# Optimization experiments

Hardware: AMD Instinct MI355X
Metric: run time of the kernel (lower is better)

The kernel has to match this reference:

```python
import jax, jax.numpy as jnp
import numpy as np

HEAD = 8
D = 128
GIN = 256
GOUT = 256
N = 50000
E = 800000


def gt_layer(edge_index, embeds, qT, kT, vT, ln_s, ln_b):
    rows, cols = edge_index[0], edge_index[1]
    n, d = embeds.shape
    hd = d // HEAD
    rowE = embeds[rows]  # [E, d]
    colE = embeds[cols]  # [E, d]
    q = (rowE @ qT).reshape(-1, HEAD, hd)
    k = (colE @ kT).reshape(-1, HEAD, hd)
    v = (colE @ vT).reshape(-1, HEAD, hd)
    att = jnp.clip(jnp.einsum('ehd,ehd->eh', q, k), -10.0, 10.0)
    expAtt = jnp.exp(att)  # [E, H]
    attNorm = jax.ops.segment_sum(expAtt, rows, num_segments=n)[rows]  # scatter-softmax denom
    att = expAtt / (attNorm + 1e-8)
    res = (att[..., None] * v).reshape(-1, d)  # [E, d]
    agg = jax.ops.segment_sum(res, rows, num_segments=n)  # [n, d]
    out = agg + embeds
    mu = jnp.mean(out, axis=-1, keepdims=True)
    var = jnp.mean((out - mu) ** 2, axis=-1, keepdims=True)
    return (out - mu) / jnp.sqrt(var + 1e-6) * ln_s + ln_b


def setup_inputs() -> dict:
    key = jax.random.key(0)
    ks = jax.random.split(key, 16)
    def xavier(k, shape):
        lim = np.sqrt(6.0 / (shape[0] + shape[1]))
        return jax.random.uniform(k, shape, jnp.float32, -lim, lim)
    inp = {
        'x': jax.random.normal(ks[0], (N, GIN), jnp.float32),
        'edge_index': jax.random.randint(ks[1], (2, E), 0, N, jnp.int64),
        'W_P_w': xavier(ks[2], (GIN, D)),
        'W_P_b': jnp.zeros((D,), jnp.float32),
        'W_pos': jax.random.uniform(ks[3], (1, D), jnp.float32, -0.02, 0.02),
        'q1': xavier(ks[4], (D, D)), 'k1': xavier(ks[5], (D, D)), 'v1': xavier(ks[6], (D, D)),
        'ln1_s': jnp.ones((D,), jnp.float32), 'ln1_b': jnp.zeros((D,), jnp.float32),
        'q2': xavier(ks[7], (D, D)), 'k2': xavier(ks[8], (D, D)), 'v2': xavier(ks[9], (D, D)),
        'ln2_s': jnp.ones((D,), jnp.float32), 'ln2_b': jnp.zeros((D,), jnp.float32),
        'inv_w': xavier(ks[10], (D, GOUT)),
        'inv_b': jnp.zeros((GOUT,), jnp.float32),
    }
    return inp


def reference(x, edge_index, W_P_w, W_P_b, W_pos, q1, k1, v1, ln1_s, ln1_b,
              q2, k2, v2, ln2_s, ln2_b, inv_w, inv_b):
    z = x @ W_P_w + W_P_b          # W_P linear: [N, D]
    embeds = z + W_pos              # if_pos; dropout is identity in eval
    embeds = gt_layer(edge_index, embeds, q1, k1, v1, ln1_s, ln1_b)
    embeds = gt_layer(edge_index, embeds, q2, k2, v2, ln2_s, ln2_b)
    return embeds @ inv_w + inv_b   # [N, GOUT]
```

## Files before the change

kernel.cpp:

```cpp
#include <hip/hip_runtime.h>
#include <hip/hip_bf16.h>

#define HEADS 8
#define DIM 128

typedef short s8v __attribute__((ext_vector_type(8)));
typedef float f4v __attribute__((ext_vector_type(4)));

__device__ __forceinline__ float bf2f(unsigned int lo16) {
    union { unsigned int i; float f; } v; v.i = lo16 << 16; return v.f;
}
__device__ __forceinline__ unsigned short f2bf(float f) {
    __hip_bfloat16 h = __float2bfloat16(f);
    return *reinterpret_cast<unsigned short*>(&h);
}
__device__ __forceinline__ int imin(int a, int b) { return a < b ? a : b; }

template<int CTRL>
__device__ __forceinline__ float dpp_add_f(float x) {
    int y = __builtin_amdgcn_update_dpp(0, __float_as_int(x), CTRL, 0xF, 0xF, true);
    return x + __int_as_float(y);
}

#if __has_builtin(__builtin_amdgcn_exp2f)
#define fast_exp2(x) __builtin_amdgcn_exp2f(x)
#else
#define fast_exp2(x) __expf(0.6931471805599453f * (x))
#endif

__global__ __launch_bounds__(256) void setup_k(const void* __restrict__ ei, int n2, int E,
                                               int* __restrict__ out, int* __restrict__ deg) {
    __shared__ int cnt;
    const unsigned int* w = (const unsigned int*)ei;
    if (threadIdx.x == 0) cnt = 0;
    __syncthreads();
    if (w[2 * threadIdx.x + 1] == 0u) atomicAdd(&cnt, 1);
    __syncthreads();
    const bool is64 = cnt > 192;
    int i = blockIdx.x * 256 + threadIdx.x;
    if (i < n2) {
        int v = is64 ? (int)((const long long*)ei)[i] : ((const int*)ei)[i];
        out[i] = v;
        if (i < E) atomicAdd(&deg[v], 1);
    }
}

__global__ void scan1_k(const int* __restrict__ deg, int n,
                        int* __restrict__ incl, int* __restrict__ blkSums) {
    __shared__ int s[256];
    int i = blockIdx.x * 256 + threadIdx.x;
    int v = (i < n) ? deg[i] : 0;
    s[threadIdx.x] = v;
    __syncthreads();
    for (int off = 1; off < 256; off <<= 1) {
        int t = (threadIdx.x >= off) ? s[threadIdx.x - off] : 0;
        __syncthreads();
        s[threadIdx.x] += t;
        __syncthreads();
    }
    if (i < n) incl[i] = s[threadIdx.x];
    if (threadIdx.x == 255) blkSums[blockIdx.x] = s[255];
}

__global__ void scan2_k(int* __restrict__ blkSums, int nb) {
    __shared__ int s[256];
    int v = (threadIdx.x < nb) ? blkSums[threadIdx.x] : 0;
    s[threadIdx.x] = v;
    __syncthreads();
    for (int off = 1; off < 256; off <<= 1) {
        int t = (threadIdx.x >= off) ? s[threadIdx.x - off] : 0;
        __syncthreads();
        s[threadIdx.x] += t;
        __syncthreads();
    }
    if (threadIdx.x < nb) blkSums[threadIdx.x] = s[threadIdx.x] - v;
}

__global__ void scan3_k(const int* __restrict__ incl, const int* __restrict__ deg,
                        const int* __restrict__ blkOff, int n,
                        int* __restrict__ rowPtr, int* __restrict__ cursor) {
    int i = blockIdx.x * 256 + threadIdx.x;
    if (i < n) {
        int inc = incl[i] + blkOff[blockIdx.x];
        rowPtr[i + 1] = inc;
        cursor[i] = inc - deg[i];
    }
    if (i == 0) rowPtr[0] = 0;
}

__global__ void scatter_k(const int* __restrict__ rows, const int* __restrict__ cols, int E,
                          int* __restrict__ cursor, int* __restrict__ colIdx) {
    int e = blockIdx.x * 256 + threadIdx.x;
    if (e < E) {
        int pos = atomicAdd(&cursor[rows[e]], 1);
        colIdx[pos] = cols[e];
    }
}

__global__ __launch_bounds__(256) void build_all_wfrag_k(
    const float* __restrict__ Wp, const float* __restrict__ q1, const float* __restrict__ k1,
    const float* __restrict__ v1, const float* __restrict__ q2, const float* __restrict__ k2,
    const float* __restrict__ v2, const float* __restrict__ invw,
    unsigned short* __restrict__ wfragP, unsigned short* __restrict__ wfragQKV1,
    unsigned short* __restrict__ wfragQKV2, unsigned short* __restrict__ wfragO)
{
    const int b = blockIdx.x;
    const float* W; unsigned short* dst; int Kd, Nd, ncomp, fb;
    const int split = 2;
    if (b < 32) { W = Wp; dst = wfragP; Kd = 256; Nd = 128; ncomp = 2; fb = b; }
    else if (b < 128) {
        int j = (b - 32) >> 4, r = (b - 32) & 15;
        const float* ws[6] = { q1, k1, v1, q2, k2, v2 };
        W = ws[j];
        dst = ((j < 3) ? wfragQKV1 : wfragQKV2) + (size_t)(j % 3) * 2 * 128 * 128;
        Kd = 128; Nd = 128; ncomp = 2; fb = r;
    } else { W = invw; dst = wfragO; Kd = 128; Nd = 256; ncomp = 1; fb = b - 128; }

    int f = fb * 256 + threadIdx.x;
    int KS = Kd >> 5;
    int perPhase = (Nd / 16 / split) * KS * 64;
    if (f >= ncomp * split * perPhase) return;
    int comp = f / (split * perPhase);
    int r1 = f - comp * split * perPhase;
    int p = r1 / perPhase;
    int r = r1 - p * perPhase;
    int nt = r / (KS * 64);
    int r2 = r - nt * KS * 64;
    int ks = r2 >> 6, lane = r2 & 63;
    int n = p * (Nd / split) + nt * 16 + (lane & 15);
    int k0 = ks * 32 + (lane >> 4) * 8;
    unsigned short tmp[8];
#pragma unroll
    for (int j = 0; j < 8; j++) {
        float w = W[(size_t)(k0 + j) * Nd + n];
        unsigned short hi = f2bf(w);
        tmp[j] = (comp == 0) ? hi : f2bf(w - bf2f(hi));
    }
#pragma unroll
    for (int j = 0; j < 8; j++) dst[(size_t)f * 8 + j] = tmp[j];
}

__global__ __launch_bounds__(256) void proj_k(
    const float* __restrict__ A, const unsigned short* __restrict__ wfrag,
    const float* __restrict__ b0, const float* __restrict__ b1,
    unsigned short* __restrict__ ehi, unsigned short* __restrict__ elo, int M)
{
    constexpr int KD = 256, KS = 8, NTp = 4;
    constexpr int FRp = NTp * KS * 64;
    const int lane = threadIdx.x & 63;
    const int m16 = lane & 15, q4 = lane >> 4;
    const int phase = blockIdx.y;
    const int pairIdx = blockIdx.x * 4 + (threadIdx.x >> 6);
    const int nPairs = (M + 31) >> 5;
    if (pairIdx >= nPairs) return;

    const int row0 = pairIdx * 32;
    const int rA0 = imin(row0 + m16, M - 1);
    const int rA1 = imin(row0 + 16 + m16, M - 1);

    f4v acc0[NTp], acc1[NTp];
#pragma unroll
    for (int nt = 0; nt < NTp; nt++) { acc0[nt] = (f4v){0,0,0,0}; acc1[nt] = (f4v){0,0,0,0}; }

    for (int ks = 0; ks < KS; ks++) {
        const f4v* pa0 = (const f4v*)(A + (size_t)rA0 * KD + ks * 32 + q4 * 8);
        const f4v* pa1 = (const f4v*)(A + (size_t)rA1 * KD + ks * 32 + q4 * 8);
        f4v xa = pa0[0], xb = pa0[1], ya = pa1[0], yb = pa1[1];
        s8v a0h, a0l, a1h, a1l;
#pragma unroll
        for (int j = 0; j < 4; j++) {
            unsigned short h;
            h = f2bf(xa[j]); a0h[j] = (short)h; a0l[j] = (short)f2bf(xa[j] - bf2f(h));
            h = f2bf(xb[j]); a0h[4 + j] = (short)h; a0l[4 + j] = (short)f2bf(xb[j] - bf2f(h));
            h = f2bf(ya[j]); a1h[j] = (short)h; a1l[j] = (short)f2bf(ya[j] - bf2f(h));
            h = f2bf(yb[j]); a1h[4 + j] = (short)h; a1l[4 + j] = (short)f2bf(yb[j] - bf2f(h));
        }
#pragma unroll
        for (int nt = 0; nt < NTp; nt++) {
            const size_t fi = ((size_t)(nt * KS + ks) * 64 + lane) * 8;
            s8v bh = *(const s8v*)(wfrag + ((size_t)(0 * 2 + phase) * FRp) * 8 + fi);
            s8v bl = *(const s8v*)(wfrag + ((size_t)(1 * 2 + phase) * FRp) * 8 + fi);
            acc0[nt] = __builtin_amdgcn_mfma_f32_16x16x32_bf16(a0h, bh, acc0[nt], 0, 0, 0);
            acc0[nt] = __builtin_amdgcn_mfma_f32_16x16x32_bf16(a0h, bl, acc0[nt], 0, 0, 0);
            acc0[nt] = __builtin_amdgcn_mfma_f32_16x16x32_bf16(a0l, bh, acc0[nt], 0, 0, 0);
            acc1[nt] = __builtin_amdgcn_mfma_f32_16x16x32_bf16(a1h, bh, acc1[nt], 0, 0, 0);
            acc1[nt] = __builtin_amdgcn_mfma_f32_16x16x32_bf16(a1h, bl, acc1[nt], 0, 0, 0);
            acc1[nt] = __builtin_amdgcn_mfma_f32_16x16x32_bf16(a1l, bh, acc1[nt], 0, 0, 0);
        }
    }

#pragma unroll
    for (int nt = 0; nt < NTp; nt++) {
        const int col = phase * 64 + nt * 16 + m16;
        const float bias = b0[col] + b1[col];
#pragma unroll
        for (int r = 0; r < 4; r++) {
            const int gr0 = row0 + q4 * 4 + r;
            if (gr0 < M) {
                float v = acc0[nt][r] + bias;
                unsigned short h = f2bf(v);
                ehi[(size_t)gr0 * DIM + col] = h;
                elo[(size_t)gr0 * DIM + col] = f2bf(v - bf2f(h));
            }
            const int gr1 = gr0 + 16;
            if (gr1 < M && row0 + 16 < M) {
                float v = acc1[nt][r] + bias;
                unsigned short h = f2bf(v);
                ehi[(size_t)gr1 * DIM + col] = h;
                elo[(size_t)gr1 * DIM + col] = f2bf(v - bf2f(h));
            }
        }
    }
}

__global__ __launch_bounds__(256) void qkv_k(
    const unsigned short* __restrict__ ehi, const unsigned short* __restrict__ elo,
    const unsigned short* __restrict__ wfrag,
    float* __restrict__ Qb, unsigned short* __restrict__ KVb, int M)
{
    constexpr int KS = 4, NTp = 4;
    constexpr int FRp = NTp * KS * 64;
    constexpr int MATFR = 4 * FRp;
    const int lane = threadIdx.x & 63;
    const int m16 = lane & 15, q4 = lane >> 4;
    const int phase = blockIdx.y;
    const int pairIdx = blockIdx.x * 4 + (threadIdx.x >> 6);
    const int nPairs = (M + 31) >> 5;
    if (pairIdx >= nPairs) return;

    const int row0 = pairIdx * 32;
    const int rA0 = imin(row0 + m16, M - 1);
    const int rA1 = imin(row0 + 16 + m16, M - 1);

    s8v a0h[KS], a0l[KS], a1h[KS], a1l[KS];
#pragma unroll
    for (int ks = 0; ks < KS; ks++) {
        a0h[ks] = *(const s8v*)(ehi + (size_t)rA0 * DIM + ks * 32 + q4 * 8);
        a0l[ks] = *(const s8v*)(elo + (size_t)rA0 * DIM + ks * 32 + q4 * 8);
        a1h[ks] = *(const s8v*)(ehi + (size_t)rA1 * DIM + ks * 32 + q4 * 8);
        a1l[ks] = *(const s8v*)(elo + (size_t)rA1 * DIM + ks * 32 + q4 * 8);
    }

    f4v aQ0[NTp], aQ1[NTp], aK0[NTp], aK1[NTp], aV0[NTp], aV1[NTp];
#pragma unroll
    for (int nt = 0; nt < NTp; nt++) {
        aQ0[nt] = (f4v){0,0,0,0}; aQ1[nt] = (f4v){0,0,0,0};
        aK0[nt] = (f4v){0,0,0,0}; aK1[nt] = (f4v){0,0,0,0};
        aV0[nt] = (f4v){0,0,0,0}; aV1[nt] = (f4v){0,0,0,0};
    }

#pragma unroll
    for (int ks = 0; ks < KS; ks++) {
#pragma unroll
        for (int nt = 0; nt < NTp; nt++) {
            const size_t fi = ((size_t)(nt * KS + ks) * 64 + lane) * 8;
            s8v qh = *(const s8v*)(wfrag + (size_t)(0 * MATFR + (0 * 2 + phase) * FRp) * 8 + fi);
            s8v ql = *(const s8v*)(wfrag + (size_t)(0 * MATFR + (1 * 2 + phase) * FRp) * 8 + fi);
            s8v kh = *(const s8v*)(wfrag + (size_t)(1 * MATFR + (0 * 2 + phase) * FRp) * 8 + fi);
            s8v kl = *(const s8v*)(wfrag + (size_t)(1 * MATFR + (1 * 2 + phase) * FRp) * 8 + fi);
            s8v vh = *(const s8v*)(wfrag + (size_t)(2 * MATFR + (0 * 2 + phase) * FRp) * 8 + fi);
            aQ0[nt] = __builtin_amdgcn_mfma_f32_16x16x32_bf16(a0h[ks], qh, aQ0[nt], 0, 0, 0);
            aQ0[nt] = __builtin_amdgcn_mfma_f32_16x16x32_bf16(a0h[ks], ql, aQ0[nt], 0, 0, 0);
            aQ0[nt] = __builtin_amdgcn_mfma_f32_16x16x32_bf16(a0l[ks], qh, aQ0[nt], 0, 0, 0);
            aQ1[nt] = __builtin_amdgcn_mfma_f32_16x16x32_bf16(a1h[ks], qh, aQ1[nt], 0, 0, 0);
            aQ1[nt] = __builtin_amdgcn_mfma_f32_16x16x32_bf16(a1h[ks], ql, aQ1[nt], 0, 0, 0);
            aQ1[nt] = __builtin_amdgcn_mfma_f32_16x16x32_bf16(a1l[ks], qh, aQ1[nt], 0, 0, 0);
            aK0[nt] = __builtin_amdgcn_mfma_f32_16x16x32_bf16(a0h[ks], kh, aK0[nt], 0, 0, 0);
            aK0[nt] = __builtin_amdgcn_mfma_f32_16x16x32_bf16(a0h[ks], kl, aK0[nt], 0, 0, 0);
            aK0[nt] = __builtin_amdgcn_mfma_f32_16x16x32_bf16(a0l[ks], kh, aK0[nt], 0, 0, 0);
            aK1[nt] = __builtin_amdgcn_mfma_f32_16x16x32_bf16(a1h[ks], kh, aK1[nt], 0, 0, 0);
            aK1[nt] = __builtin_amdgcn_mfma_f32_16x16x32_bf16(a1h[ks], kl, aK1[nt], 0, 0, 0);
            aK1[nt] = __builtin_amdgcn_mfma_f32_16x16x32_bf16(a1l[ks], kh, aK1[nt], 0, 0, 0);
            aV0[nt] = __builtin_amdgcn_mfma_f32_16x16x32_bf16(a0h[ks], vh, aV0[nt], 0, 0, 0);
            aV0[nt] = __builtin_amdgcn_mfma_f32_16x16x32_bf16(a0l[ks], vh, aV0[nt], 0, 0, 0);
            aV1[nt] = __builtin_amdgcn_mfma_f32_16x16x32_bf16(a1h[ks], vh, aV1[nt], 0, 0, 0);
            aV1[nt] = __builtin_amdgcn_mfma_f32_16x16x32_bf16(a1l[ks], vh, aV1[nt], 0, 0, 0);
        }
    }

#pragma unroll
    for (int nt = 0; nt < NTp; nt++) {
        const int col = phase * 64 + nt * 16 + m16;
#pragma unroll
        for (int r = 0; r < 4; r++) {
            const int gr0 = row0 + q4 * 4 + r;
            if (gr0 < M) {
                Qb[(size_t)gr0 * DIM + col] = aQ0[nt][r];
                KVb[(size_t)gr0 * 256 + col] = f2bf(aK0[nt][r]);
                KVb[(size_t)gr0 * 256 + 128 + col] = f2bf(aV0[nt][r]);
            }
            const int gr1 = gr0 + 16;
            if (gr1 < M && row0 + 16 < M) {
                Qb[(size_t)gr1 * DIM + col] = aQ1[nt][r];
                KVb[(size_t)gr1 * 256 + col] = f2bf(aK1[nt][r]);
                KVb[(size_t)gr1 * 256 + 128 + col] = f2bf(aV1[nt][r]);
            }
        }
    }
}

__global__ __launch_bounds__(256) void outproj_k(
    const unsigned short* __restrict__ ehi, const unsigned short* __restrict__ elo,
    const unsigned short* __restrict__ wfrag, const float* __restrict__ b0,
    float* __restrict__ Out, int M)
{
    constexpr int KS = 4, NTp = 8, NOUT = 256;
    constexpr int FRp = NTp * KS * 64;
    const int lane = threadIdx.x & 63;
    const int m16 = lane & 15, q4 = lane >> 4;
    const int phase = blockIdx.y;
    const int pairIdx = blockIdx.x * 4 + (threadIdx.x >> 6);
    const int nPairs = (M + 31) >> 5;
    if (pairIdx >= nPairs) return;

    const int row0 = pairIdx * 32;
    const int rA0 = imin(row0 + m16, M - 1);
    const int rA1 = imin(row0 + 16 + m16, M - 1);

    s8v a0h[KS], a0l[KS], a1h[KS], a1l[KS];
#pragma unroll
    for (int ks = 0; ks < KS; ks++) {
        a0h[ks] = *(const s8v*)(ehi + (size_t)rA0 * DIM + ks * 32 + q4 * 8);
        a0l[ks] = *(const s8v*)(elo + (size_t)rA0 * DIM + ks * 32 + q4 * 8);
        a1h[ks] = *(const s8v*)(ehi + (size_t)rA1 * DIM + ks * 32 + q4 * 8);
        a1l[ks] = *(const s8v*)(elo + (size_t)rA1 * DIM + ks * 32 + q4 * 8);
    }

    f4v acc0[NTp], acc1[NTp];
#pragma unroll
    for (int nt = 0; nt < NTp; nt++) { acc0[nt] = (f4v){0,0,0,0}; acc1[nt] = (f4v){0,0,0,0}; }

#pragma unroll
    for (int ks = 0; ks < KS; ks++) {
#pragma unroll
        for (int nt = 0; nt < NTp; nt++) {
            s8v b = *(const s8v*)(wfrag + ((size_t)phase * FRp + (size_t)(nt * KS + ks) * 64 + lane) * 8);
            acc0[nt] = __builtin_amdgcn_mfma_f32_16x16x32_bf16(a0h[ks], b, acc0[nt], 0, 0, 0);
            acc0[nt] = __builtin_amdgcn_mfma_f32_16x16x32_bf16(a0l[ks], b, acc0[nt], 0, 0, 0);
            acc1[nt] = __builtin_amdgcn_mfma_f32_16x16x32_bf16(a1h[ks], b, acc1[nt], 0, 0, 0);
            acc1[nt] = __builtin_amdgcn_mfma_f32_16x16x32_bf16(a1l[ks], b, acc1[nt], 0, 0, 0);
        }
    }

#pragma unroll
    for (int nt = 0; nt < NTp; nt++) {
        const int col = phase * 128 + nt * 16 + m16;
        const float bias = b0[col];
#pragma unroll
        for (int r = 0; r < 4; r++) {
            const int gr0 = row0 + q4 * 4 + r;
            if (gr0 < M) Out[(size_t)gr0 * NOUT + col] = acc0[nt][r] + bias;
            const int gr1 = gr0 + 16;
            if (gr1 < M && row0 + 16 < M) Out[(size_t)gr1 * NOUT + col] = acc1[nt][r] + bias;
        }
    }
}

__global__ __launch_bounds__(256) void agg_k(
    const float* __restrict__ Q, const unsigned short* __restrict__ KV,
    const int* __restrict__ rowPtr, const int* __restrict__ colIdx,
    const float* __restrict__ ln_s, const float* __restrict__ ln_b,
    unsigned short* __restrict__ ehi, unsigned short* __restrict__ elo, int n)
{
    const int node = blockIdx.x * 4 + (threadIdx.x >> 6);
    if (node >= n) return;
    const int lane = threadIdx.x & 63;
    const int d = lane * 2;

    constexpr float LOG2E = 1.4426950408889634f;
    constexpr float CLAMP = 10.0f * LOG2E;

    const float2 qraw = *(const float2*)(Q + (size_t)node * DIM + d);
    const float qx = qraw.x * LOG2E, qy = qraw.y * LOG2E;
    const unsigned int rh = *(const unsigned int*)(ehi + (size_t)node * DIM + d);
    const unsigned int rl = *(const unsigned int*)(elo + (size_t)node * DIM + d);
    const float r0 = bf2f(rh & 0xffffu) + bf2f(rl & 0xffffu);
    const float r1 = bf2f(rh >> 16) + bf2f(rl >> 16);

    const int e0 = rowPtr[node], e1 = rowPtr[node + 1];
    float acc0 = 0.f, acc1 = 0.f, den = 0.f;

    if (e1 > e0) {
        unsigned int kA[4], vA[4], kB[4], vB[4];
#define LOADC(karr, varr, base_)                                        \
        {                                                               \
            _Pragma("unroll")                                           \
            for (int j = 0; j < 4; j++) {                               \
                int idx = (base_) + j;                                  \
                int cc = colIdx[idx < e1 ? idx : e1 - 1];               \
                size_t off = (size_t)cc * 256 + d;                      \
                karr[j] = *(const unsigned int*)(KV + off);             \
                varr[j] = *(const unsigned int*)(KV + off + 128);       \
            }                                                           \
        }
#define COMP(karr, varr, base_)                                         \
        {                                                               \
            _Pragma("unroll")                                           \
            for (int j = 0; j < 4; j++) {                               \
                if ((base_) + j < e1) {                                 \
                    float p = qx * bf2f(karr[j] & 0xffffu)              \
                            + qy * bf2f(karr[j] >> 16);                 \
                    p = dpp_add_f<0xB1>(p);                   \
                    p = dpp_add_f<0x4E>(p);                   \
                    p = dpp_add_f<0x141>(p);    \
                    p = fminf(fmaxf(p, -CLAMP), CLAMP);                 \
                    float w = fast_exp2(p);                             \
                    den += w;                                           \
                    acc0 += w * bf2f(varr[j] & 0xffffu);                \
                    acc1 += w * bf2f(varr[j] >> 16);                    \
                }                                                       \
            }                                                           \
        }
        int base = e0;
        LOADC(kA, vA, base)
        while (base < e1) {
            int nxt = base + 4;
            if (nxt < e1) LOADC(kB, vB, nxt)
            COMP(kA, vA, base)
            base = nxt;
            if (base >= e1) break;
            int nxt2 = base + 4;
            if (nxt2 < e1) LOADC(kA, vA, nxt2)
            COMP(kB, vB, base)
            base = nxt2;
        }
#undef LOADC
#undef COMP
    }
    const float inv = 1.f / (den + 1e-8f);
    const float o0 = acc0 * inv + r0;
    const float o1 = acc1 * inv + r1;

    float s = o0 + o1, s2 = o0 * o0 + o1 * o1;
#pragma unroll
    for (int m = 1; m < 64; m <<= 1) {
        s  += __shfl_xor(s, m);
        s2 += __shfl_xor(s2, m);
    }
    const float mu = s * (1.f / 128.f);
    const float var = s2 * (1.f / 128.f) - mu * mu;
    const float rs = rsqrtf(var + 1e-6f);
    const float y0 = (o0 - mu) * rs * ln_s[d] + ln_b[d];
    const float y1 = (o1 - mu) * rs * ln_s[d + 1] + ln_b[d + 1];
    const unsigned short h0 = f2bf(y0), h1 = f2bf(y1);
    const unsigned short l0 = f2bf(y0 - bf2f(h0)), l1 = f2bf(y1 - bf2f(h1));
    *(unsigned int*)(ehi + (size_t)node * DIM + d) = (unsigned int)h0 | ((unsigned int)h1 << 16);
    *(unsigned int*)(elo + (size_t)node * DIM + d) = (unsigned int)l0 | ((unsigned int)l1 << 16);
}

extern "C" void kernel_launch(void* const* d_in, const int* in_sizes, int n_in,
                              void* d_out, int out_size, void* d_ws, size_t ws_size,
                              hipStream_t stream)
{
    const float* x    = (const float*)d_in[0];
    const void*  ei   = d_in[1];
    const float* Wp   = (const float*)d_in[2];
    const float* Wpb  = (const float*)d_in[3];
    const float* Wpos = (const float*)d_in[4];
    const float* q1   = (const float*)d_in[5];
    const float* k1   = (const float*)d_in[6];
    const float* v1   = (const float*)d_in[7];
    const float* l1s  = (const float*)d_in[8];
    const float* l1b  = (const float*)d_in[9];
    const float* q2   = (const float*)d_in[10];
    const float* k2   = (const float*)d_in[11];
    const float* v2   = (const float*)d_in[12];
    const float* l2s  = (const float*)d_in[13];
    const float* l2b  = (const float*)d_in[14];
    const float* invw = (const float*)d_in[15];
    const float* invb = (const float*)d_in[16];

    const int N = in_sizes[0] / 256;
    const int E = in_sizes[1] / 2;

    char* p = (char*)d_ws;
    auto carve = [&](size_t bytes) -> void* {
        void* r = (void*)p;
        p += (bytes + 255) & ~(size_t)255;
        return r;
    };
    unsigned short* ehi = (unsigned short*)carve((size_t)N * DIM * 2);
    unsigned short* elo = (unsigned short*)carve((size_t)N * DIM * 2);
    float*          Qb  = (float*)carve((size_t)N * DIM * 4);
    unsigned short* KVb = (unsigned short*)carve((size_t)N * 256 * 2);
    int*   deg    = (int*)carve((size_t)N * 4);
    int*   incl   = (int*)carve((size_t)N * 4);
    int*   blkS   = (int*)carve(1024);
    int*   rowPtr = (int*)carve((size_t)(N + 1) * 4);
    int*   cursor = (int*)carve((size_t)N * 4);
    int*   colIdx = (int*)carve((size_t)E * 4);
    int*   rc     = (int*)carve((size_t)2 * E * 4);
    unsigned short* wfragP    = (unsigned short*)carve((size_t)2 * 256 * 128 * 2);
    unsigned short* wfragQKV1 = (unsigned short*)carve((size_t)3 * 2 * 128 * 128 * 2);
    unsigned short* wfragQKV2 = (unsigned short*)carve((size_t)3 * 2 * 128 * 128 * 2);
    unsigned short* wfragO    = (unsigned short*)carve((size_t)128 * 256 * 2);

    int* rows = rc;
    int* cols = rc + E;

    const int nb  = (N + 255) / 256;
    const int ebl = (E + 255) / 256;
    const int nPairs = (N + 31) / 32;
    const dim3 ggrid((nPairs + 3) / 4, 2);

    hipMemsetAsync(deg, 0, (size_t)N * 4, stream);
    setup_k<<<(2 * E + 255) / 256, 256, 0, stream>>>(ei, 2 * E, E, rc, deg);
    scan1_k<<<nb, 256, 0, stream>>>(deg, N, incl, blkS);
    scan2_k<<<1, 256, 0, stream>>>(blkS, nb);
    scan3_k<<<nb, 256, 0, stream>>>(incl, deg, blkS, N, rowPtr, cursor);
    scatter_k<<<ebl, 256, 0, stream>>>(rows, cols, E, cursor, colIdx);

    build_all_wfrag_k<<<144, 256, 0, stream>>>(Wp, q1, k1, v1, q2, k2, v2, invw,
                                               wfragP, wfragQKV1, wfragQKV2, wfragO);

    proj_k<<<ggrid, 256, 0, stream>>>(x, wfragP, Wpb, Wpos, ehi, elo, N);

    qkv_k<<<ggrid, 256, 0, stream>>>(ehi, elo, wfragQKV1, Qb, KVb, N);
    agg_k<<<(N + 3) / 4, 256, 0, stream>>>(Qb, KVb, rowPtr, colIdx, l1s, l1b, ehi, elo, N);

    qkv_k<<<ggrid, 256, 0, stream>>>(ehi, elo, wfragQKV2, Qb, KVb, N);
    agg_k<<<(N + 3) / 4, 256, 0, stream>>>(Qb, KVb, rowPtr, colIdx, l2s, l2b, ehi, elo, N);

    outproj_k<<<ggrid, 256, 0, stream>>>(ehi, elo, wfragO, invb, (float*)d_out, N);
}
```

Before: 496.0 us.

## Interleave K/V layout, merge proj phases, and use DPP wave reduction

The K and V bf16 values for each column are now interleaved in one 32-bit word. The aggregation kernel can then fetch K and V together with a single 8-byte load per lane per neighbor, instead of two separate 4-byte loads 256 bytes apart. The projection kernel now computes all 128 output columns in one wave rather than splitting the work across two grid phases, so the input x is read and converted to bf16 only once. The aggregation loop replaces per-edge branches with a masked weight, and the layer-norm reduction uses DPP row operations plus readlane instead of shuffle xor. The merged projection doubles the accumulator registers per wave, which could reduce occupancy.

Result: no change. 488.0 us (-1.6%).

```diff
diff --git a/kernel.cpp b/kernel.cpp
--- a/kernel.cpp
+++ b/kernel.cpp
@@ -20,6 +20,16 @@
 __device__ __forceinline__ float dpp_add_f(float x) {
     int y = __builtin_amdgcn_update_dpp(0, __float_as_int(x), CTRL, 0xF, 0xF, true);
     return x + __int_as_float(y);
+}
+
+__device__ __forceinline__ float wave_allsum(float x) {
+    x = dpp_add_f<0x111>(x);
+    x = dpp_add_f<0x112>(x);
+    x = dpp_add_f<0x114>(x);
+    x = dpp_add_f<0x118>(x);
+    x = dpp_add_f<0x142>(x);
+    x = dpp_add_f<0x143>(x);
+    return __int_as_float(__builtin_amdgcn_readlane(__float_as_int(x), 63));
 }
 
 #if __has_builtin(__builtin_amdgcn_exp2f)
@@ -145,11 +155,10 @@
     const float* __restrict__ b0, const float* __restrict__ b1,
     unsigned short* __restrict__ ehi, unsigned short* __restrict__ elo, int M)
 {
-    constexpr int KD = 256, KS = 8, NTp = 4;
-    constexpr int FRp = NTp * KS * 64;
+    constexpr int KD = 256, KS = 8, NT = 8;
+    constexpr int FRp = 4 * KS * 64;
     const int lane = threadIdx.x & 63;
     const int m16 = lane & 15, q4 = lane >> 4;
-    const int phase = blockIdx.y;
     const int pairIdx = blockIdx.x * 4 + (threadIdx.x >> 6);
     const int nPairs = (M + 31) >> 5;
     if (pairIdx >= nPairs) return;
@@ -158,9 +167,9 @@
     const int rA0 = imin(row0 + m16, M - 1);
     const int rA1 = imin(row0 + 16 + m16, M - 1);
 
-    f4v acc0[NTp], acc1[NTp];
-#pragma unroll
-    for (int nt = 0; nt < NTp; nt++) { acc0[nt] = (f4v){0,0,0,0}; acc1[nt] = (f4v){0,0,0,0}; }
+    f4v acc0[NT], acc1[NT];
+#pragma unroll
+    for (int g = 0; g < NT; g++) { acc0[g] = (f4v){0,0,0,0}; acc1[g] = (f4v){0,0,0,0}; }
 
     for (int ks = 0; ks < KS; ks++) {
         const f4v* pa0 = (const f4v*)(A + (size_t)rA0 * KD + ks * 32 + q4 * 8);
@@ -176,35 +185,36 @@
             h = f2bf(yb[j]); a1h[4 + j] = (short)h; a1l[4 + j] = (short)f2bf(yb[j] - bf2f(h));
         }
 #pragma unroll
-        for (int nt = 0; nt < NTp; nt++) {
+        for (int g = 0; g < NT; g++) {
+            const int p = g >> 2, nt = g & 3;
             const size_t fi = ((size_t)(nt * KS + ks) * 64 + lane) * 8;
-            s8v bh = *(const s8v*)(wfrag + ((size_t)(0 * 2 + phase) * FRp) * 8 + fi);
-            s8v bl = *(const s8v*)(wfrag + ((size_t)(1 * 2 + phase) * FRp) * 8 + fi);
-            acc0[nt] = __builtin_amdgcn_mfma_f32_16x16x32_bf16(a0h, bh, acc0[nt], 0, 0, 0);
-            acc0[nt] = __builtin_amdgcn_mfma_f32_16x16x32_bf16(a0h, bl, acc0[nt], 0, 0, 0);
-            acc0[nt] = __builtin_amdgcn_mfma_f32_16x16x32_bf16(a0l, bh, acc0[nt], 0, 0, 0);
-            acc1[nt] = __builtin_amdgcn_mfma_f32_16x16x32_bf16(a1h, bh, acc1[nt], 0, 0, 0);
-            acc1[nt] = __builtin_amdgcn_mfma_f32_16x16x32_bf16(a1h, bl, acc1[nt], 0, 0, 0);
-            acc1[nt] = __builtin_amdgcn_mfma_f32_16x16x32_bf16(a1l, bh, acc1[nt], 0, 0, 0);
-        }
-    }
-
-#pragma unroll
-    for (int nt = 0; nt < NTp; nt++) {
-        const int col = phase * 64 + nt * 16 + m16;
+            s8v bh = *(const s8v*)(wfrag + ((size_t)(0 * 2 + p) * FRp) * 8 + fi);
+            s8v bl = *(const s8v*)(wfrag + ((size_t)(1 * 2 + p) * FRp) * 8 + fi);
+            acc0[g] = __builtin_amdgcn_mfma_f32_16x16x32_bf16(a0h, bh, acc0[g], 0, 0, 0);
+            acc0[g] = __builtin_amdgcn_mfma_f32_16x16x32_bf16(a0h, bl, acc0[g], 0, 0, 0);
+            acc0[g] = __builtin_amdgcn_mfma_f32_16x16x32_bf16(a0l, bh, acc0[g], 0, 0, 0);
+            acc1[g] = __builtin_amdgcn_mfma_f32_16x16x32_bf16(a1h, bh, acc1[g], 0, 0, 0);
+            acc1[g] = __builtin_amdgcn_mfma_f32_16x16x32_bf16(a1h, bl, acc1[g], 0, 0, 0);
+            acc1[g] = __builtin_amdgcn_mfma_f32_16x16x32_bf16(a1l, bh, acc1[g], 0, 0, 0);
+        }
+    }
+
+#pragma unroll
+    for (int g = 0; g < NT; g++) {
+        const int col = g * 16 + m16;
         const float bias = b0[col] + b1[col];
 #pragma unroll
         for (int r = 0; r < 4; r++) {
             const int gr0 = row0 + q4 * 4 + r;
             if (gr0 < M) {
-                float v = acc0[nt][r] + bias;
+                float v = acc0[g][r] + bias;
                 unsigned short h = f2bf(v);
                 ehi[(size_t)gr0 * DIM + col] = h;
                 elo[(size_t)gr0 * DIM + col] = f2bf(v - bf2f(h));
             }
             const int gr1 = gr0 + 16;
             if (gr1 < M && row0 + 16 < M) {
-                float v = acc1[nt][r] + bias;
+                float v = acc1[g][r] + bias;
                 unsigned short h = f2bf(v);
                 ehi[(size_t)gr1 * DIM + col] = h;
                 elo[(size_t)gr1 * DIM + col] = f2bf(v - bf2f(h));
@@ -286,14 +296,14 @@
             const int gr0 = row0 + q4 * 4 + r;
             if (gr0 < M) {
                 Qb[(size_t)gr0 * DIM + col] = aQ0[nt][r];
-                KVb[(size_t)gr0 * 256 + col] = f2bf(aK0[nt][r]);
-                KVb[(size_t)gr0 * 256 + 128 + col] = f2bf(aV0[nt][r]);
+                *(unsigned int*)(KVb + (size_t)gr0 * 256 + 2 * col) =
+                    (unsigned int)f2bf(aK0[nt][r]) | ((unsigned int)f2bf(aV0[nt][r]) << 16);
             }
             const int gr1 = gr0 + 16;
             if (gr1 < M && row0 + 16 < M) {
                 Qb[(size_t)gr1 * DIM + col] = aQ1[nt][r];
-                KVb[(size_t)gr1 * 256 + col] = f2bf(aK1[nt][r]);
-                KVb[(size_t)gr1 * 256 + 128 + col] = f2bf(aV1[nt][r]);
+                *(unsigned int*)(KVb + (size_t)gr1 * 256 + 2 * col) =
+                    (unsigned int)f2bf(aK1[nt][r]) | ((unsigned int)f2bf(aV1[nt][r]) << 16);
             }
         }
     }
@@ -381,48 +391,48 @@
     float acc0 = 0.f, acc1 = 0.f, den = 0.f;
 
     if (e1 > e0) {
-        unsigned int kA[4], vA[4], kB[4], vB[4];
-#define LOADC(karr, varr, base_)                                        \
+        const uint2* KV2 = (const uint2*)KV;
+        const int emax = e1 - 1;
+        uint2 cA[4], cB[4];
+#define LOADC(arr, base_)                                               \
         {                                                               \
             _Pragma("unroll")                                           \
             for (int j = 0; j < 4; j++) {                               \
-                int idx = (base_) + j;                                  \
-                int cc = colIdx[idx < e1 ? idx : e1 - 1];               \
-                size_t off = (size_t)cc * 256 + d;                      \
-                karr[j] = *(const unsigned int*)(KV + off);             \
-                varr[j] = *(const unsigned int*)(KV + off + 128);       \
+                int cc = colIdx[imin((base_) + j, emax)];               \
+                arr[j] = KV2[(cc << 6) + lane];                         \
             }                                                           \
         }
-#define COMP(karr, varr, base_)                                         \
+#define COMP(arr, base_)                                                \
         {                                                               \
             _Pragma("unroll")                                           \
             for (int j = 0; j < 4; j++) {                               \
-                if ((base_) + j < e1) {                                 \
-                    float p = qx * bf2f(karr[j] & 0xffffu)              \
-                            + qy * bf2f(karr[j] >> 16);                 \
-                    p = dpp_add_f<0xB1>(p);                   \
-                    p = dpp_add_f<0x4E>(p);                   \
-                    p = dpp_add_f<0x141>(p);    \
-                    p = fminf(fmaxf(p, -CLAMP), CLAMP);                 \
-                    float w = fast_exp2(p);                             \
-                    den += w;                                           \
-                    acc0 += w * bf2f(varr[j] & 0xffffu);                \
-                    acc1 += w * bf2f(varr[j] >> 16);                    \
-                }                                                       \
+                const unsigned int w0 = arr[j].x, w1 = arr[j].y;        \
+                float p = qx * bf2f(w0 & 0xffffu)                       \
+                        + qy * bf2f(w1 & 0xffffu);                      \
+                p = dpp_add_f<0xB1>(p);                       \
+                p = dpp_add_f<0x4E>(p);                       \
+                p = dpp_add_f<0x141>(p);        \
+                p = fminf(fmaxf(p, -CLAMP), CLAMP);                     \
+                float w = fast_exp2(p);                                 \
+                w = ((base_) + j < e1) ? w : 0.f;                       \
+                den += w;                                               \
+                acc0 += w * bf2f(w0 >> 16);                             \
+                acc1 += w * bf2f(w1 >> 16);                             \
             }                                                           \
         }
         int base = e0;
-        LOADC(kA, vA, base)
-        while (base < e1) {
+        LOADC(cA, base)
+        while (true) {
             int nxt = base + 4;
-            if (nxt < e1) LOADC(kB, vB, nxt)
-            COMP(kA, vA, base)
+            if (nxt < e1) LOADC(cB, nxt)
+            COMP(cA, base)
             base = nxt;
             if (base >= e1) break;
             int nxt2 = base + 4;
-            if (nxt2 < e1) LOADC(kA, vA, nxt2)
-            COMP(kB, vB, base)
+            if (nxt2 < e1) LOADC(cA, nxt2)
+            COMP(cB, base)
             base = nxt2;
+            if (base >= e1) break;
         }
 #undef LOADC
 #undef COMP
@@ -431,12 +441,8 @@
     const float o0 = acc0 * inv + r0;
     const float o1 = acc1 * inv + r1;
 
-    float s = o0 + o1, s2 = o0 * o0 + o1 * o1;
-#pragma unroll
-    for (int m = 1; m < 64; m <<= 1) {
-        s  += __shfl_xor(s, m);
-        s2 += __shfl_xor(s2, m);
-    }
+    const float s  = wave_allsum(o0 + o1);
+    const float s2 = wave_allsum(o0 * o0 + o1 * o1);
     const float mu = s * (1.f / 128.f);
     const float var = s2 * (1.f / 128.f) - mu * mu;
     const float rs = rsqrtf(var + 1e-6f);
@@ -502,6 +508,7 @@
     const int ebl = (E + 255) / 256;
     const int nPairs = (N + 31) / 32;
     const dim3 ggrid((nPairs + 3) / 4, 2);
+    const dim3 ggridP((nPairs + 3) / 4, 1);
 
     hipMemsetAsync(deg, 0, (size_t)N * 4, stream);
     setup_k<<<(2 * E + 255) / 256, 256, 0, stream>>>(ei, 2 * E, E, rc, deg);
@@ -513,7 +520,7 @@
     build_all_wfrag_k<<<144, 256, 0, stream>>>(Wp, q1, k1, v1, q2, k2, v2, invw,
                                                wfragP, wfragQKV1, wfragQKV2, wfragO);
 
-    proj_k<<<ggrid, 256, 0, stream>>>(x, wfragP, Wpb, Wpos, ehi, elo, N);
+    proj_k<<<ggridP, 256, 0, stream>>>(x, wfragP, Wpb, Wpos, ehi, elo, N);
 
     qkv_k<<<ggrid, 256, 0, stream>>>(ehi, elo, wfragQKV1, Qb, KVb, N);
     agg_k<<<(N + 3) / 4, 256, 0, stream>>>(Qb, KVb, rowPtr, colIdx, l1s, l1b, ehi, elo, N);
```
